# Kernel optimization log

Measured on AMD Instinct MI355X. Metric: run time of the kernel, lower is better.

## Reference

```python
import jax, jax.numpy as jnp
import numpy as np

B, H_IMG, W_IMG = 2, 192, 192
DIM, HEADS, WS, SHIFT = 192, 6, 8, 4
MLP_HID = 4 * DIM
EPS = 1e-5


def _rel_pos_index(ws):
    coords = np.stack(np.meshgrid(np.arange(ws), np.arange(ws), indexing='ij'))  # (2, ws, ws)
    cf = coords.reshape(2, -1)
    rel = (cf[:, :, None] - cf[:, None, :]).transpose(1, 2, 0)  # (ww, ww, 2)
    rel[:, :, 0] += ws - 1
    rel[:, :, 1] += ws - 1
    rel[:, :, 0] *= 2 * ws - 1
    return jnp.asarray(rel.sum(-1))  # (ww, ww) int


def _attn_mask(h, w, ws, shift):
    img = np.zeros((h, w))
    cnt = 0
    for hs in (slice(0, -ws), slice(-ws, -shift), slice(-shift, None)):
        for wsl in (slice(0, -ws), slice(-ws, -shift), slice(-shift, None)):
            img[hs, wsl] = cnt
            cnt += 1
    mw = img.reshape(h // ws, ws, w // ws, ws).transpose(0, 2, 1, 3).reshape(-1, ws * ws)
    am = mw[:, None, :] - mw[:, :, None]
    return jnp.asarray(np.where(am != 0, -100.0, 0.0), dtype=jnp.float32)


def setup_inputs() -> dict:
    key = jax.random.key(0)
    ks = jax.random.split(key, 16)
    n = H_IMG * W_IMG
    std = 0.02
    inp = {
        'x_left': jax.random.normal(ks[0], (B, n, DIM), jnp.float32),
        'x_right': jax.random.normal(ks[1], (B, n, DIM), jnp.float32),
        'd_left': jax.random.uniform(ks[2], (B, H_IMG, W_IMG), jnp.float32) * 8.0,
        'd_right': jax.random.uniform(ks[3], (B, H_IMG, W_IMG), jnp.float32) * 8.0,
        'norm1_g': jnp.ones((DIM,), jnp.float32),
        'norm1_b': jnp.zeros((DIM,), jnp.float32),
        'q_w': jax.random.normal(ks[4], (DIM, DIM), jnp.float32) * std,
        'q_b': jnp.zeros((DIM,), jnp.float32),
        'kv_w': jax.random.normal(ks[5], (DIM, 2 * DIM), jnp.float32) * std,
        'kv_b': jnp.zeros((2 * DIM,), jnp.float32),
        'proj_w': jax.random.normal(ks[6], (DIM, DIM), jnp.float32) * std,
        'proj_b': jnp.zeros((DIM,), jnp.float32),
        'rel_bias_table': jax.random.normal(ks[7], ((2 * WS - 1) ** 2, HEADS), jnp.float32) * std,
        'norm2_g': jnp.ones((DIM,), jnp.float32),
        'norm2_b': jnp.zeros((DIM,), jnp.float32),
        'fc1_w': jax.random.normal(ks[8], (DIM, MLP_HID), jnp.float32) * std,
        'fc1_b': jnp.zeros((MLP_HID,), jnp.float32),
        'fc2_w': jax.random.normal(ks[9], (MLP_HID, DIM), jnp.float32) * std,
        'fc2_b': jnp.zeros((DIM,), jnp.float32),
        'h': H_IMG,
        'w': W_IMG,
    }
    return inp


def _forward(x_left, x_right, d_left, d_right,
             norm1_g, norm1_b, q_w, q_b, kv_w, kv_b, proj_w, proj_b,
             rel_bias_table, norm2_g, norm2_b, fc1_w, fc1_b, fc2_w, fc2_b,
             h, w):
    b, n, c = x_left.shape
    ws, shift, heads = WS, SHIFT, HEADS
    hd = c // heads
    scale = hd ** -0.5
    ww = ws * ws
    nW = (h // ws) * (w // ws)

    rel_idx = _rel_pos_index(ws)
    # (heads, ww, ww) gathered relative-position bias
    bias = rel_bias_table[rel_idx.reshape(-1)].reshape(ww, ww, heads).transpose(2, 0, 1)
    mask = _attn_mask(h, w, ws, shift)  # (nW, ww, ww)

    coords_w = jnp.arange(w, dtype=jnp.float32)[None, None, :]
    r2l = jnp.clip(coords_w + 0.5 - d_left, 0.0, None).astype(jnp.int32)
    l2r = jnp.clip(coords_w + 0.5 + d_right, None, float(w - 1)).astype(jnp.int32)

    def ln(x, g, bt):
        mu = x.mean(-1, keepdims=True)
        var = ((x - mu) ** 2).mean(-1, keepdims=True)
        return (x - mu) / jnp.sqrt(var + EPS) * g + bt

    sc_l, sc_r = x_left, x_right
    xl = ln(x_left, norm1_g, norm1_b).reshape(b, h, w, c)
    xr = ln(x_right, norm1_g, norm1_b).reshape(b, h, w, c)
    # epipolar gather along width
    xl_sel = jnp.take_along_axis(xl, l2r[..., None], axis=2)
    xr_sel = jnp.take_along_axis(xr, r2l[..., None], axis=2)

    def shift_f(x):
        return jnp.roll(x, (-shift, -shift), axis=(1, 2))

    def part(x):  # window partition -> (b*nW, ww, c)
        x = x.reshape(b, h // ws, ws, w // ws, ws, c).transpose(0, 1, 3, 2, 4, 5)
        return x.reshape(-1, ww, c)

    xlw, xrw = part(shift_f(xl)), part(shift_f(xr))
    xlsw, xrsw = part(shift_f(xl_sel)), part(shift_f(xr_sel))

    def win_attn(xq, xkv):
        B_ = xq.shape[0]
        q = (xq @ q_w + q_b).reshape(B_, ww, heads, hd).transpose(0, 2, 1, 3) * scale
        kv = (xkv @ kv_w + kv_b).reshape(B_, ww, 2, heads, hd).transpose(2, 0, 3, 1, 4)
        k, v = kv[0], kv[1]
        a = jnp.einsum('bhqd,bhkd->bhqk', q, k) + bias[None]
        a = a.reshape(B_ // nW, nW, heads, ww, ww) + mask[None, :, None]
        a = jax.nn.softmax(a.reshape(B_, heads, ww, ww), axis=-1)
        o = jnp.einsum('bhqk,bhkd->bqhd', a, v).reshape(B_, ww, c)
        return o @ proj_w + proj_b, a

    xlT, a_r2l = win_attn(xlw, xrsw)
    xrT, a_l2r = win_attn(xrw, xlsw)

    def m_relax(M, p=2):  # sum over +-p shifts along the query axis
        out = M
        for i in range(1, p + 1):
            out = out + jnp.pad(M[:, :, :-i, :], ((0, 0), (0, 0), (i, 0), (0, 0)))
            out = out + jnp.pad(M[:, :, i:, :], ((0, 0), (0, 0), (0, i), (0, 0)))
        return out

    m_l = jnp.einsum('bhik,bhki->bhi', m_relax(a_r2l), a_l2r)
    m_r = jnp.einsum('bhik,bhki->bhi', m_relax(a_l2r), a_r2l)
    m_l = jax.lax.stop_gradient(jnp.tanh(5.0 * m_l.transpose(0, 2, 1)[..., None]))  # (B_, ww, heads, 1)
    m_r = jax.lax.stop_gradient(jnp.tanh(5.0 * m_r.transpose(0, 2, 1)[..., None]))

    def fuse(x_orig, x_t, m):
        B_ = x_orig.shape[0]
        xo = x_orig.reshape(B_, ww, heads, hd)
        xt = x_t.reshape(B_, ww, heads, hd)
        return (xo * (1.0 - m) + xt * m).reshape(B_, ww, c)

    xlT = fuse(xlw, xlT, m_l)
    xrT = fuse(xrw, xrT, m_r)

    def rev(win):  # window reverse + roll back
        x = win.reshape(b, h // ws, w // ws, ws, ws, c).transpose(0, 1, 3, 2, 4, 5).reshape(b, h, w, c)
        return jnp.roll(x, (shift, shift), axis=(1, 2))

    xl_out = sc_l + rev(xlT).reshape(b, n, c)
    xr_out = sc_r + rev(xrT).reshape(b, n, c)

    def mlp(x):
        return jax.nn.gelu(x @ fc1_w + fc1_b, approximate=False) @ fc2_w + fc2_b

    xl_out = xl_out + mlp(ln(xl_out, norm2_g, norm2_b))
    xr_out = xr_out + mlp(ln(xr_out, norm2_g, norm2_b))
    return xl_out, xr_out


def reference(x_left, x_right, d_left, d_right,
              norm1_g, norm1_b, q_w, q_b, kv_w, kv_b, proj_w, proj_b,
              rel_bias_table, norm2_g, norm2_b, fc1_w, fc1_b, fc2_w, fc2_b,
              h, w):
    return _forward(x_left, x_right, d_left, d_right,
                    norm1_g, norm1_b, q_w, q_b, kv_w, kv_b, proj_w, proj_b,
                    rel_bias_table, norm2_g, norm2_b, fc1_w, fc1_b, fc2_w, fc2_b,
                    h, w)
```

## Files before the change

kernel.cpp:

```cpp
#include <hip/hip_runtime.h>
#include <hip/hip_bf16.h>

#define BB 2
#define HH 192
#define WIMG 192
#define CC 192
#define NHEADS 6
#define HD 32
#define NTOK (HH*WIMG)
#define NWX 24
#define NWIN 576
#define BWIN (BB*NWIN)
#define MLPH 768
#define EPS_ 1e-5f
#define NSIDE_TOK (BB*NTOK)

typedef __attribute__((ext_vector_type(8))) short bf16x8;
typedef __attribute__((ext_vector_type(4))) float f32x4;

#define GLOBAL_AS __attribute__((address_space(1)))
#define LDS_AS __attribute__((address_space(3)))
__device__ __forceinline__ void gll16(const void* g, void* l) {
    __builtin_amdgcn_global_load_lds((const GLOBAL_AS unsigned int*)g,
                                     (LDS_AS unsigned int*)l, 16, 0, 0);
}

__device__ __forceinline__ unsigned short f2bf(float f) {
    __hip_bfloat16 h = __float2bfloat16(f);
    return *reinterpret_cast<unsigned short*>(&h);
}
__device__ __forceinline__ float bfu(unsigned short u) {
    return __uint_as_float(((unsigned int)u) << 16);
}
__device__ __forceinline__ float gelu_fast(float x) {
    float z = 1.5957691216f*(x + 0.044715f*x*x*x);
    float e = __expf(z);
    float t = 1.0f - 2.0f/(e + 1.0f);
    return 0.5f*x*(1.0f + t);
}
__device__ __forceinline__ int tokof(int b, int wi, int wj, int p) {
    int rh = wi*8 + (p>>3), rw = wj*8 + (p&7);
    int i = rh + 4; if (i >= HH) i -= HH;
    int j = rw + 4; if (j >= WIMG) j -= WIMG;
    return b*NTOK + i*WIMG + j;
}

__global__ __launch_bounds__(256) void ln1_kernel(
    const float* __restrict__ xl, const float* __restrict__ xr,
    const float* __restrict__ g, const float* __restrict__ bta,
    __hip_bfloat16* __restrict__ xln_all)
{
    int token = blockIdx.x*4 + (threadIdx.x >> 6);
    int lane = threadIdx.x & 63;
    const float* src;
    __hip_bfloat16* dst;
    if (token < NSIDE_TOK) { src = xl + (size_t)token*CC; dst = xln_all + (size_t)token*CC; }
    else { int t2 = token - NSIDE_TOK; src = xr + (size_t)t2*CC; dst = xln_all + (size_t)token*CC; }
    float v0 = src[lane], v1 = src[lane+64], v2 = src[lane+128];
    float s = v0+v1+v2;
    float q = v0*v0 + v1*v1 + v2*v2;
    #pragma unroll
    for (int m = 32; m; m >>= 1) { s += __shfl_xor(s, m, 64); q += __shfl_xor(q, m, 64); }
    float mu = s * (1.0f/CC);
    float inv = rsqrtf(fmaxf(q*(1.0f/CC) - mu*mu, 0.0f) + EPS_);
    dst[lane]     = __float2bfloat16((v0-mu)*inv*g[lane]     + bta[lane]);
    dst[lane+64]  = __float2bfloat16((v1-mu)*inv*g[lane+64]  + bta[lane+64]);
    dst[lane+128] = __float2bfloat16((v2-mu)*inv*g[lane+128] + bta[lane+128]);
}

__global__ __launch_bounds__(256) void map_kernel(
    const float* __restrict__ d_left, const float* __restrict__ d_right,
    int* __restrict__ map)
{
    int gid = blockIdx.x*256 + threadIdx.x;
    int side = (gid >= NSIDE_TOK) ? 1 : 0;
    int row = gid - side*NSIDE_TOK;
    int j = row % WIMG;
    float d = side ? d_right[row] : d_left[row];
    int jj;
    if (!side) { float f = (float)j + 0.5f - d; f = fmaxf(f, 0.f); jj = (int)f; }
    else       { float f = (float)j + 0.5f + d; f = fminf(f, 191.f); jj = (int)f; }
    map[gid] = (side ? 0 : NSIDE_TOK) + row - j + jj;
}

__global__ __launch_bounds__(256) void conv_w_kernel(
    const float* __restrict__ q_w, const float* __restrict__ kv_w,
    const float* __restrict__ proj_w, const float* __restrict__ fc1_w,
    const float* __restrict__ fc2_w,
    __hip_bfloat16* __restrict__ q_wf, __hip_bfloat16* __restrict__ kv_wf,
    __hip_bfloat16* __restrict__ proj_f, __hip_bfloat16* __restrict__ W1f,
    __hip_bfloat16* __restrict__ W2f)
{
    int idx = blockIdx.x*256 + threadIdx.x;
    if (idx < 36864) {
        int j = idx & 7, lane = (idx>>3) & 63, fr = idx>>9;
        int ct = fr % 12, ks = fr / 12;
        int n = ct*16 + (lane&15), k = ks*32 + (lane>>4)*8 + j;
        q_wf[idx] = __float2bfloat16(q_w[(size_t)k*192 + n]);
    } else if (idx < 110592) {
        int i2 = idx - 36864;
        int j = i2 & 7, lane = (i2>>3) & 63, fr = i2>>9;
        int ct = fr % 24, ks = fr / 24;
        int n = ct*16 + (lane&15), k = ks*32 + (lane>>4)*8 + j;
        kv_wf[i2] = __float2bfloat16(kv_w[(size_t)k*384 + n]);
    } else if (idx < 147456) {
        int i2 = idx - 110592;
        int j = i2 & 7, lane = (i2>>3) & 63, fr = i2>>9;
        int ct = fr % 12, h = fr / 12;
        int n = ct*16 + (lane&15), k = h*32 + (lane>>4)*8 + j;
        proj_f[i2] = __float2bfloat16(proj_w[(size_t)k*192 + n]);
    } else if (idx < 294912) {
        int i2 = idx - 147456;
        int j = i2 & 7, lane = (i2>>3) & 63, fr = i2>>9;
        int ct = fr & 1, ks = (fr>>1) % 6, cc2 = fr / 12;
        int n = cc2*32 + ct*16 + (lane&15), k = ks*32 + (lane>>4)*8 + j;
        W1f[i2] = __float2bfloat16(fc1_w[(size_t)k*MLPH + n]);
    } else {
        int i2 = idx - 294912;
        int j = i2 & 7, lane = (i2>>3) & 63, fr = i2>>9;
        int ct = fr % 12, ks = (fr/12) % 2, cc = fr / 24;
        int n = ct*16 + (lane&15), k = cc*64 + ks*32 + (lane>>4)*8 + j;
        W2f[i2] = __float2bfloat16(fc2_w[(size_t)k*192 + n]);
    }
}

__global__ __launch_bounds__(256) void bias_setup_kernel(
    const float* __restrict__ table, float* __restrict__ bias_glob)
{
    int idx = blockIdx.x*256 + threadIdx.x;
    int h = idx >> 12, rem = idx & 4095;
    int q = rem >> 6, k = rem & 63;
    int qy = q>>3, qx = q&7, ky = k>>3, kx = k&7;
    int ridx = (qy-ky+7)*15 + (qx-kx+7);
    bias_glob[idx] = table[ridx*NHEADS + h];
}

template<int NT>
__global__ __launch_bounds__(256) void proj_gemm_kernel(
    const __hip_bfloat16* __restrict__ in, const __hip_bfloat16* __restrict__ Wf,
    const float* __restrict__ bias, const int* __restrict__ map,
    __hip_bfloat16* __restrict__ outp, float scale)
{
    __shared__ unsigned short wst[2][NT*512];
    const int tid = threadIdx.x, lane = tid & 63, w = tid >> 6;
    const int r16 = lane & 15, kg = lane >> 4, w16 = w*16;
    const size_t baserow = (size_t)blockIdx.x * 64;
    const int row = (int)baserow + w16 + r16;
    const size_t arow = map ? (size_t)map[row] : (size_t)row;

    bf16x8 aReg[6];
    #pragma unroll
    for (int ks = 0; ks < 6; ++ks)
        aReg[ks] = *reinterpret_cast<const bf16x8*>(in + arow*CC + ks*32 + kg*8);

    const char* wsrc = (const char*)Wf;
    const int soff = w*1024 + lane*16;
    #pragma unroll
    for (int i = 0; i < NT/4; ++i)
        gll16(wsrc + i*4096 + soff, (char*)wst[0] + i*4096 + w*1024);

    f32x4 acc[NT];
    #pragma unroll
    for (int ct = 0; ct < NT; ++ct) { float bv = bias[ct*16+r16]; acc[ct] = (f32x4){bv,bv,bv,bv}; }

    #pragma unroll
    for (int ks = 0; ks < 6; ++ks) {
        __syncthreads();
        if (ks < 5) {
            const char* s2 = wsrc + (size_t)(ks+1)*NT*1024;
            #pragma unroll
            for (int i = 0; i < NT/4; ++i)
                gll16(s2 + i*4096 + soff, (char*)wst[(ks+1)&1] + i*4096 + w*1024);
        }
        #pragma unroll
        for (int ct = 0; ct < NT; ++ct) {
            bf16x8 bb = *reinterpret_cast<const bf16x8*>(wst[ks&1] + ct*512 + lane*8);
            acc[ct] = __builtin_amdgcn_mfma_f32_16x16x32_bf16(aReg[ks], bb, acc[ct], 0, 0, 0);
        }
    }
    const int ldo = NT*16;
    #pragma unroll
    for (int ct = 0; ct < NT; ++ct)
        #pragma unroll
        for (int r = 0; r < 4; ++r)
            outp[(baserow + w16 + kg*4 + r)*ldo + ct*16 + r16] =
                __float2bfloat16(acc[ct][r] * scale);
}

__global__ __launch_bounds__(128) void attn_pm_kernel(
    const __hip_bfloat16* __restrict__ Qglob,
    const __hip_bfloat16* __restrict__ KVglob,
    const float* __restrict__ bias_glob,
    __hip_bfloat16* __restrict__ Og,
    float* __restrict__ mg)
{
    __shared__ unsigned short Pl[2][64*72];
    __shared__ unsigned short Vl[2][32*72];
    const int tid = threadIdx.x, lane = tid & 63, s = tid >> 6;
    const int r16 = lane & 15, kg = lane >> 4;
    const int bid = blockIdx.x;
    const int wd = bid / NHEADS, h = bid % NHEADS;
    const int b = wd / NWIN, win = wd % NWIN;
    const int wi = win / NWX, wj = win % NWX;
    const bool edge_i = (wi == NWX-1), edge_j = (wj == NWX-1);

    const __hip_bfloat16* Qs  = Qglob  + (size_t)s*NSIDE_TOK*CC;
    const __hip_bfloat16* KVs = KVglob + (size_t)s*NSIDE_TOK*(2*CC);

    int tokQ[4];
    #pragma unroll
    for (int mi = 0; mi < 4; ++mi) tokQ[mi] = tokof(b, wi, wj, mi*16 + r16);
    const int tokV = tokof(b, wi, wj, lane);

    unsigned short* P = Pl[s];
    unsigned short* V = Vl[s];

    {
        bf16x8 vv[4];
        #pragma unroll
        for (int dg = 0; dg < 4; ++dg)
            vv[dg] = *reinterpret_cast<const bf16x8*>(
                KVs + (size_t)tokV*(2*CC) + CC + h*HD + dg*8);
        #pragma unroll
        for (int dg = 0; dg < 4; ++dg)
            #pragma unroll
            for (int jj = 0; jj < 8; ++jj)
                V[(dg*8+jj)*72 + lane] = (unsigned short)vv[dg][jj];
    }

    bf16x8 aQ[4], bK[4];
    #pragma unroll
    for (int mi = 0; mi < 4; ++mi)
        aQ[mi] = *reinterpret_cast<const bf16x8*>(
            Qs + (size_t)tokQ[mi]*CC + h*HD + kg*8);
    #pragma unroll
    for (int ni = 0; ni < 4; ++ni)
        bK[ni] = *reinterpret_cast<const bf16x8*>(
            KVs + (size_t)tokQ[ni]*(2*CC) + h*HD + kg*8);
    f32x4 S[4][4];
    #pragma unroll
    for (int mi = 0; mi < 4; ++mi)
        #pragma unroll
        for (int ni = 0; ni < 4; ++ni)
            S[mi][ni] = __builtin_amdgcn_mfma_f32_16x16x32_bf16(
                aQ[mi], bK[ni], (f32x4){0.f,0.f,0.f,0.f}, 0, 0, 0);

    #pragma unroll
    for (int mi = 0; mi < 4; ++mi)
        #pragma unroll
        for (int ni = 0; ni < 4; ++ni)
            #pragma unroll
            for (int rr = 0; rr < 4; ++rr) {
                int q = mi*16 + kg*4 + rr, k = ni*16 + r16;
                float bm = bias_glob[h*4096 + q*64 + k];
                int qy = q>>3, qx = q&7, ky = k>>3, kx = k&7;
                bool msk = (edge_i && ((qy<4) != (ky<4))) ||
                           (edge_j && ((qx<4) != (kx<4)));
                S[mi][ni][rr] += bm + (msk ? -100.0f : 0.0f);
            }

    float mx[4][4], sm[4][4];
    #pragma unroll
    for (int mi = 0; mi < 4; ++mi)
        #pragma unroll
        for (int rr = 0; rr < 4; ++rr)
            mx[mi][rr] = fmaxf(fmaxf(S[mi][0][rr], S[mi][1][rr]),
                               fmaxf(S[mi][2][rr], S[mi][3][rr]));
    #pragma unroll
    for (int m = 1; m <= 8; m <<= 1)
        #pragma unroll
        for (int mi = 0; mi < 4; ++mi)
            #pragma unroll
            for (int rr = 0; rr < 4; ++rr)
                mx[mi][rr] = fmaxf(mx[mi][rr], __shfl_xor(mx[mi][rr], m, 64));
    #pragma unroll
    for (int mi = 0; mi < 4; ++mi)
        #pragma unroll
        for (int rr = 0; rr < 4; ++rr) sm[mi][rr] = 0.f;
    #pragma unroll
    for (int mi = 0; mi < 4; ++mi)
        #pragma unroll
        for (int ni = 0; ni < 4; ++ni)
            #pragma unroll
            for (int rr = 0; rr < 4; ++rr) {
                S[mi][ni][rr] = __expf(S[mi][ni][rr] - mx[mi][rr]);
                sm[mi][rr] += S[mi][ni][rr];
            }
    #pragma unroll
    for (int m = 1; m <= 8; m <<= 1)
        #pragma unroll
        for (int mi = 0; mi < 4; ++mi)
            #pragma unroll
            for (int rr = 0; rr < 4; ++rr)
                sm[mi][rr] += __shfl_xor(sm[mi][rr], m, 64);
    #pragma unroll
    for (int mi = 0; mi < 4; ++mi)
        #pragma unroll
        for (int rr = 0; rr < 4; ++rr) sm[mi][rr] = 1.0f / sm[mi][rr];

    #pragma unroll
    for (int mi = 0; mi < 4; ++mi)
        #pragma unroll
        for (int ni = 0; ni < 4; ++ni)
            #pragma unroll
            for (int rr = 0; rr < 4; ++rr)
                P[(mi*16 + kg*4 + rr)*72 + ni*16 + r16] =
                    f2bf(S[mi][ni][rr] * sm[mi][rr]);

    {
        f32x4 O[4][2];
        #pragma unroll
        for (int mi = 0; mi < 4; ++mi)
            #pragma unroll
            for (int dt = 0; dt < 2; ++dt) O[mi][dt] = (f32x4){0.f,0.f,0.f,0.f};
        #pragma unroll
        for (int ks = 0; ks < 2; ++ks) {
            bf16x8 aP[4], bV[2];
            #pragma unroll
            for (int mi = 0; mi < 4; ++mi)
                aP[mi] = *reinterpret_cast<const bf16x8*>(
                    P + (mi*16 + r16)*72 + ks*32 + kg*8);
            #pragma unroll
            for (int dt = 0; dt < 2; ++dt)
                bV[dt] = *reinterpret_cast<const bf16x8*>(
                    V + (dt*16 + r16)*72 + ks*32 + kg*8);
            #pragma unroll
            for (int mi = 0; mi < 4; ++mi)
                #pragma unroll
                for (int dt = 0; dt < 2; ++dt)
                    O[mi][dt] = __builtin_amdgcn_mfma_f32_16x16x32_bf16(
                        aP[mi], bV[dt], O[mi][dt], 0, 0, 0);
        }
        __hip_bfloat16* ob = Og + ((size_t)(s*BWIN + wd)*64)*CC + h*HD;
        #pragma unroll
        for (int mi = 0; mi < 4; ++mi)
            #pragma unroll
            for (int dt = 0; dt < 2; ++dt)
                #pragma unroll
                for (int rr = 0; rr < 4; ++rr)
                    ob[(size_t)(mi*16 + kg*4 + rr)*CC + dt*16 + r16] =
                        __float2bfloat16(O[mi][dt][rr]);
    }

    __syncthreads();

    {
        const unsigned short* Pa = Pl[s];
        const unsigned short* Pb = Pl[s^1];
        const int i = lane;
        const int s0 = (i >= 2) ? -2 : -i;
        const int s1 = (i <= 61) ? 2 : 63 - i;
        float acc = 0.f;
        for (int k = 0; k < 64; k += 2) {
            float pb0 = bfu(Pb[k*72 + i]);
            float pb1 = bfu(Pb[(k+1)*72 + i]);
            float a0 = 0.f, a1 = 0.f;
            for (int ss = s0; ss <= s1; ++ss) {
                unsigned int pr = *reinterpret_cast<const unsigned int*>(
                    &Pa[(i+ss)*72 + k]);
                a0 += bfu((unsigned short)(pr & 0xffff));
                a1 += bfu((unsigned short)(pr >> 16));
            }
            acc += a0*pb0 + a1*pb1;
        }
        float e = __expf(10.0f * acc);
        mg[((size_t)(s*BWIN + wd)*NHEADS + h)*64 + i] = 1.0f - 2.0f/(e + 1.0f);
    }
}

__global__ __launch_bounds__(256) void projfuse_kernel(
    const __hip_bfloat16* __restrict__ Og,
    const __hip_bfloat16* __restrict__ proj_f,
    const float* __restrict__ proj_b,
    const float* __restrict__ mg,
    const __hip_bfloat16* __restrict__ xln_all,
    const float* __restrict__ x_left, const float* __restrict__ x_right,
    const float* __restrict__ g2, const float* __restrict__ b2,
    float* __restrict__ out, __hip_bfloat16* __restrict__ xln2)
{
    __shared__ unsigned short wst[2][12*512];
    const int tid = threadIdx.x, lane = tid & 63, w = tid >> 6;
    const int r16 = lane & 15, kg = lane >> 4, w16 = w*16;
    const int bid = blockIdx.x;
    const int s = bid / BWIN, wd = bid % BWIN;
    const int b = wd / NWIN, win = wd % NWIN;
    const int wi = win / NWX, wj = win % NWX;

    const size_t orow = (size_t)(s*BWIN + wd)*64 + w16 + r16;
    bf16x8 aReg[6];
    #pragma unroll
    for (int ks = 0; ks < 6; ++ks)
        aReg[ks] = *reinterpret_cast<const bf16x8*>(Og + orow*CC + ks*32 + kg*8);

    const char* wsrc = (const char*)proj_f;
    const int soff = w*1024 + lane*16;
    #pragma unroll
    for (int i = 0; i < 3; ++i)
        gll16(wsrc + i*4096 + soff, (char*)wst[0] + i*4096 + w*1024);

    f32x4 acc[12];
    #pragma unroll
    for (int ct = 0; ct < 12; ++ct) { float bv = proj_b[ct*16+r16]; acc[ct] = (f32x4){bv,bv,bv,bv}; }

    #pragma unroll
    for (int ks = 0; ks < 6; ++ks) {
        __syncthreads();
        if (ks < 5) {
            const char* s2 = wsrc + (size_t)(ks+1)*12288;
            #pragma unroll
            for (int i = 0; i < 3; ++i)
                gll16(s2 + i*4096 + soff, (char*)wst[(ks+1)&1] + i*4096 + w*1024);
        }
        #pragma unroll
        for (int ct = 0; ct < 12; ++ct) {
            bf16x8 bb = *reinterpret_cast<const bf16x8*>(wst[ks&1] + ct*512 + lane*8);
            acc[ct] = __builtin_amdgcn_mfma_f32_16x16x32_bf16(aReg[ks], bb, acc[ct], 0, 0, 0);
        }
    }

    int tk[4];
    #pragma unroll
    for (int rr = 0; rr < 4; ++rr) tk[rr] = tokof(b, wi, wj, w16 + kg*4 + rr);
    const float* xo_s = s ? x_right : x_left;
    const __hip_bfloat16* xw_s = xln_all + (size_t)s*NSIDE_TOK*CC;
    float* out_s = out + (size_t)s*NSIDE_TOK*CC;
    __hip_bfloat16* xln2_s = xln2 + (size_t)s*NSIDE_TOK*CC;
    const float* mrow = mg + (size_t)(s*BWIN + wd)*NHEADS*64;

    float g2c[12], b2c[12];
    #pragma unroll
    for (int ct = 0; ct < 12; ++ct) {
        g2c[ct] = g2[ct*16 + r16];
        b2c[ct] = b2[ct*16 + r16];
    }

    #pragma unroll
    for (int ct = 0; ct < 12; ++ct) {
        int col = ct*16 + r16;
        int h = ct >> 1;
        #pragma unroll
        for (int rr = 0; rr < 4; ++rr) {
            int q = w16 + kg*4 + rr;
            size_t tt = (size_t)tk[rr];
            float m = mrow[h*64 + q];
            float xw = __bfloat162float(xw_s[tt*CC + col]);
            float p = acc[ct][rr];
            float val = xo_s[tt*CC + col] + xw + (p - xw)*m;
            out_s[tt*CC + col] = val;
            acc[ct][rr] = val;
        }
    }

    #pragma unroll
    for (int rr = 0; rr < 4; ++rr) {
        float sum = 0.f, sq = 0.f;
        #pragma unroll
        for (int ct = 0; ct < 12; ++ct) {
            float v = acc[ct][rr];
            sum += v; sq += v*v;
        }
        #pragma unroll
        for (int m = 1; m <= 8; m <<= 1) {
            sum += __shfl_xor(sum, m, 64);
            sq  += __shfl_xor(sq,  m, 64);
        }
        float mu = sum * (1.0f/CC);
        float inv = rsqrtf(fmaxf(sq*(1.0f/CC) - mu*mu, 0.0f) + EPS_);
        size_t tt = (size_t)tk[rr];
        #pragma unroll
        for (int ct = 0; ct < 12; ++ct) {
            unsigned short uv = f2bf((acc[ct][rr]-mu)*inv*g2c[ct] + b2c[ct]);
            *reinterpret_cast<unsigned short*>(&xln2_s[tt*CC + ct*16 + r16]) = uv;
        }
    }
}

__global__ __launch_bounds__(512) void mlp_mfma_kernel(
    float* __restrict__ out, const __hip_bfloat16* __restrict__ xln2,
    const __hip_bfloat16* __restrict__ W1f, const float* __restrict__ fc1_b,
    const __hip_bfloat16* __restrict__ W2f, const float* __restrict__ fc2_b)
{
    __shared__ unsigned short hbuf[2][64*72];
    __shared__ unsigned short wst[2][6144];
    const int tid  = threadIdx.x;
    const int lane = tid & 63;
    const int w    = tid >> 6;
    const int tg   = w >> 2;
    const int w4   = w & 3;
    const int r16 = lane & 15, kg = lane >> 4, w16 = w4*16;
    const size_t base = (size_t)blockIdx.x * 128 * CC + (size_t)tg * 64 * CC;

    bf16x8 aReg[6];
    #pragma unroll
    for (int ks = 0; ks < 6; ++ks)
        aReg[ks] = *reinterpret_cast<const bf16x8*>(
            xln2 + base + (size_t)(w16 + r16)*CC + ks*32 + kg*8);

    const char* W1c = (const char*)W1f;
    const char* W2c = (const char*)W2f;
    const int soff = w*4096 + lane*16;
    const int doff = w*4096;
    unsigned short* hb = hbuf[tg];

    if (w < 3) {
        #pragma unroll
        for (int i = 0; i < 4; ++i)
            gll16(W1c + i*1024 + soff, (char*)wst[0] + i*1024 + doff);
    }

    f32x4 acc2[12];
    #pragma unroll
    for (int i = 0; i < 12; ++i) acc2[i] = (f32x4){0.f,0.f,0.f,0.f};

    for (int cc = 0; cc < 12; ++cc) {
        f32x4 acc1[4];
        __builtin_amdgcn_s_barrier();
        if (w < 3) {
            const char* s2 = W1c + (size_t)(2*cc+1)*12288;
            #pragma unroll
            for (int i = 0; i < 4; ++i)
                gll16(s2 + i*1024 + soff, (char*)wst[1] + i*1024 + doff);
        }
        asm volatile("s_waitcnt vmcnt(4)" ::: "memory");
        __builtin_amdgcn_s_barrier();
        #pragma unroll
        for (int c2 = 0; c2 < 2; ++c2) {
            float bv = fc1_b[cc*64 + c2*16 + r16];
            acc1[c2] = (f32x4){bv,bv,bv,bv};
        }
        #pragma unroll
        for (int ks = 0; ks < 6; ++ks)
            #pragma unroll
            for (int c2 = 0; c2 < 2; ++c2) {
                bf16x8 bw = *reinterpret_cast<const bf16x8*>(wst[0] + (ks*2+c2)*512 + lane*8);
                acc1[c2] = __builtin_amdgcn_mfma_f32_16x16x32_bf16(aReg[ks], bw, acc1[c2], 0, 0, 0);
            }
        __builtin_amdgcn_s_barrier();
        if (w < 3) {
            const char* s2 = W2c + (size_t)(2*cc)*12288;
            #pragma unroll
            for (int i = 0; i < 4; ++i)
                gll16(s2 + i*1024 + soff, (char*)wst[0] + i*1024 + doff);
        }
        asm volatile("s_waitcnt vmcnt(4)" ::: "memory");
        __builtin_amdgcn_s_barrier();
        #pragma unroll
        for (int c2 = 0; c2 < 2; ++c2) {
            float bv = fc1_b[cc*64 + 32 + c2*16 + r16];
            acc1[2+c2] = (f32x4){bv,bv,bv,bv};
        }
        #pragma unroll
        for (int ks = 0; ks < 6; ++ks)
            #pragma unroll
            for (int c2 = 0; c2 < 2; ++c2) {
                bf16x8 bw = *reinterpret_cast<const bf16x8*>(wst[1] + (ks*2+c2)*512 + lane*8);
                acc1[2+c2] = __builtin_amdgcn_mfma_f32_16x16x32_bf16(aReg[ks], bw, acc1[2+c2], 0, 0, 0);
            }
        #pragma unroll
        for (int ct = 0; ct < 4; ++ct)
            #pragma unroll
            for (int r = 0; r < 4; ++r)
                hb[(w16 + kg*4 + r)*72 + ct*16 + r16] = f2bf(gelu_fast(acc1[ct][r]));
        __builtin_amdgcn_s_barrier();
        if (w < 3) {
            const char* s2 = W2c + (size_t)(2*cc+1)*12288;
            #pragma unroll
            for (int i = 0; i < 4; ++i)
                gll16(s2 + i*1024 + soff, (char*)wst[1] + i*1024 + doff);
        }
        asm volatile("s_waitcnt vmcnt(4)" ::: "memory");
        __builtin_amdgcn_s_barrier();
        {
            bf16x8 aP = *reinterpret_cast<const bf16x8*>(hb + (w16+r16)*72 + kg*8);
            #pragma unroll
            for (int ct = 0; ct < 12; ++ct) {
                bf16x8 bw = *reinterpret_cast<const bf16x8*>(wst[0] + ct*512 + lane*8);
                acc2[ct] = __builtin_amdgcn_mfma_f32_16x16x32_bf16(aP, bw, acc2[ct], 0, 0, 0);
            }
        }
        __builtin_amdgcn_s_barrier();
        if (cc < 11) {
            if (w < 3) {
                const char* s2 = W1c + (size_t)(2*cc+2)*12288;
                #pragma unroll
                for (int i = 0; i < 4; ++i)
                    gll16(s2 + i*1024 + soff, (char*)wst[0] + i*1024 + doff);
            }
            asm volatile("s_waitcnt vmcnt(4)" ::: "memory");
        } else {
            asm volatile("s_waitcnt vmcnt(0)" ::: "memory");
        }
        __builtin_amdgcn_s_barrier();
        {
            bf16x8 aP = *reinterpret_cast<const bf16x8*>(hb + (w16+r16)*72 + 32 + kg*8);
            #pragma unroll
            for (int ct = 0; ct < 12; ++ct) {
                bf16x8 bw = *reinterpret_cast<const bf16x8*>(wst[1] + ct*512 + lane*8);
                acc2[ct] = __builtin_amdgcn_mfma_f32_16x16x32_bf16(aP, bw, acc2[ct], 0, 0, 0);
            }
        }
    }

    #pragma unroll
    for (int ct = 0; ct < 12; ++ct) {
        int col = ct*16 + r16;
        float bv = fc2_b[col];
        #pragma unroll
        for (int r = 0; r < 4; ++r) {
            size_t idx = base + (size_t)(w16 + kg*4 + r)*CC + col;
            out[idx] = out[idx] + acc2[ct][r] + bv;
        }
    }
}

extern "C" void kernel_launch(void* const* d_in, const int* in_sizes, int n_in,
                              void* d_out, int out_size, void* d_ws, size_t ws_size,
                              hipStream_t stream)
{
    (void)in_sizes; (void)n_in; (void)out_size; (void)ws_size;
    const float* x_left  = (const float*)d_in[0];
    const float* x_right = (const float*)d_in[1];
    const float* d_left  = (const float*)d_in[2];
    const float* d_right = (const float*)d_in[3];
    const float* n1g = (const float*)d_in[4];
    const float* n1b = (const float*)d_in[5];
    const float* q_w = (const float*)d_in[6];
    const float* q_b = (const float*)d_in[7];
    const float* kv_w = (const float*)d_in[8];
    const float* kv_b = (const float*)d_in[9];
    const float* proj_w = (const float*)d_in[10];
    const float* proj_b = (const float*)d_in[11];
    const float* bias_table = (const float*)d_in[12];
    const float* n2g = (const float*)d_in[13];
    const float* n2b = (const float*)d_in[14];
    const float* fc1_w = (const float*)d_in[15];
    const float* fc1_b = (const float*)d_in[16];
    const float* fc2_w = (const float*)d_in[17];
    const float* fc2_b = (const float*)d_in[18];
    float* out = (float*)d_out;

    char* ws = (char*)d_ws;
    __hip_bfloat16* xln_all  = (__hip_bfloat16*)(ws);
    __hip_bfloat16* Qg       = (__hip_bfloat16*)(ws + 56623104);
    __hip_bfloat16* KVg      = (__hip_bfloat16*)(ws + 113246208);
    __hip_bfloat16* xln2     = (__hip_bfloat16*)(ws + 113246208);
    __hip_bfloat16* q_wf     = (__hip_bfloat16*)(ws + 226492416);
    __hip_bfloat16* kv_wf    = (__hip_bfloat16*)(ws + 226566144);
    __hip_bfloat16* proj_f   = (__hip_bfloat16*)(ws + 226713600);
    __hip_bfloat16* W1f      = (__hip_bfloat16*)(ws + 226787328);
    __hip_bfloat16* W2f      = (__hip_bfloat16*)(ws + 227082240);
    float*          bias_g   = (float*)         (ws + 227377152);
    __hip_bfloat16* Og       = (__hip_bfloat16*)(ws + 227770368);
    int*            map      = (int*)           (ws + 284393472);
    float*          mg       = (float*)         (ws + 284983296);

    ln1_kernel<<<(2*NSIDE_TOK)/4, 256, 0, stream>>>(x_left, x_right, n1g, n1b, xln_all);

    conv_w_kernel<<<1728, 256, 0, stream>>>(q_w, kv_w, proj_w, fc1_w, fc2_w,
                                            q_wf, kv_wf, proj_f, W1f, W2f);
    bias_setup_kernel<<<96, 256, 0, stream>>>(bias_table, bias_g);
    map_kernel<<<(2*NSIDE_TOK)/256, 256, 0, stream>>>(d_left, d_right, map);

    proj_gemm_kernel<24><<<(2*NSIDE_TOK)/64, 256, 0, stream>>>(
        xln_all, kv_wf, kv_b, map, KVg, 1.0f);
    proj_gemm_kernel<12><<<(2*NSIDE_TOK)/64, 256, 0, stream>>>(
        xln_all, q_wf, q_b, nullptr, Qg, 0.17677669529663687f);

    attn_pm_kernel<<<BWIN*NHEADS, 128, 0, stream>>>(Qg, KVg, bias_g, Og, mg);

    projfuse_kernel<<<2*BWIN, 256, 0, stream>>>(
        Og, proj_f, proj_b, mg, xln_all, x_left, x_right, n2g, n2b, out, xln2);

    mlp_mfma_kernel<<<(2*NSIDE_TOK)/128, 512, 0, stream>>>(
        out, xln2, W1f, fc1_b, W2f, fc2_b);
}
```

Measured before the change: 536.9 us.

## Merge setup kernels, widen Q-proj and projfuse blocks, restructure attention loads

Folds the weight conversion, bias-table expansion and disparity map kernels into one setup launch to cut launch overhead. Adds a 512-thread Q projection GEMM and widens projfuse to 512 threads, so one staged weight tile in LDS serves two row groups. In both, only three waves issue the LDS loads and explicit vmcnt waits with split barriers replace __syncthreads. The attention kernel interleaves K loads with the MFMAs to lower register pressure, at the cost of being more sensitive to load latency.

```diff
diff --git a/kernel.cpp b/kernel.cpp
--- a/kernel.cpp
+++ b/kernel.cpp
@@ -68,28 +68,15 @@
     dst[lane+128] = __float2bfloat16((v2-mu)*inv*g[lane+128] + bta[lane+128]);
 }
 
-__global__ __launch_bounds__(256) void map_kernel(
-    const float* __restrict__ d_left, const float* __restrict__ d_right,
-    int* __restrict__ map)
-{
-    int gid = blockIdx.x*256 + threadIdx.x;
-    int side = (gid >= NSIDE_TOK) ? 1 : 0;
-    int row = gid - side*NSIDE_TOK;
-    int j = row % WIMG;
-    float d = side ? d_right[row] : d_left[row];
-    int jj;
-    if (!side) { float f = (float)j + 0.5f - d; f = fmaxf(f, 0.f); jj = (int)f; }
-    else       { float f = (float)j + 0.5f + d; f = fminf(f, 191.f); jj = (int)f; }
-    map[gid] = (side ? 0 : NSIDE_TOK) + row - j + jj;
-}
-
-__global__ __launch_bounds__(256) void conv_w_kernel(
+__global__ __launch_bounds__(256) void setup_kernel(
     const float* __restrict__ q_w, const float* __restrict__ kv_w,
     const float* __restrict__ proj_w, const float* __restrict__ fc1_w,
-    const float* __restrict__ fc2_w,
+    const float* __restrict__ fc2_w, const float* __restrict__ table,
+    const float* __restrict__ d_left, const float* __restrict__ d_right,
     __hip_bfloat16* __restrict__ q_wf, __hip_bfloat16* __restrict__ kv_wf,
     __hip_bfloat16* __restrict__ proj_f, __hip_bfloat16* __restrict__ W1f,
-    __hip_bfloat16* __restrict__ W2f)
+    __hip_bfloat16* __restrict__ W2f, float* __restrict__ bias_glob,
+    int* __restrict__ map)
 {
     int idx = blockIdx.x*256 + threadIdx.x;
     if (idx < 36864) {
@@ -115,24 +102,30 @@
         int ct = fr & 1, ks = (fr>>1) % 6, cc2 = fr / 12;
         int n = cc2*32 + ct*16 + (lane&15), k = ks*32 + (lane>>4)*8 + j;
         W1f[i2] = __float2bfloat16(fc1_w[(size_t)k*MLPH + n]);
-    } else {
+    } else if (idx < 442368) {
         int i2 = idx - 294912;
         int j = i2 & 7, lane = (i2>>3) & 63, fr = i2>>9;
         int ct = fr % 12, ks = (fr/12) % 2, cc = fr / 24;
         int n = ct*16 + (lane&15), k = cc*64 + ks*32 + (lane>>4)*8 + j;
         W2f[i2] = __float2bfloat16(fc2_w[(size_t)k*192 + n]);
-    }
-}
-
-__global__ __launch_bounds__(256) void bias_setup_kernel(
-    const float* __restrict__ table, float* __restrict__ bias_glob)
-{
-    int idx = blockIdx.x*256 + threadIdx.x;
-    int h = idx >> 12, rem = idx & 4095;
-    int q = rem >> 6, k = rem & 63;
-    int qy = q>>3, qx = q&7, ky = k>>3, kx = k&7;
-    int ridx = (qy-ky+7)*15 + (qx-kx+7);
-    bias_glob[idx] = table[ridx*NHEADS + h];
+    } else if (idx < 466944) {
+        int i3 = idx - 442368;
+        int h = i3 >> 12, rem = i3 & 4095;
+        int q = rem >> 6, k = rem & 63;
+        int qy = q>>3, qx = q&7, ky = k>>3, kx = k&7;
+        int ridx = (qy-ky+7)*15 + (qx-kx+7);
+        bias_glob[i3] = table[ridx*NHEADS + h];
+    } else {
+        int gid = idx - 466944;
+        int side = (gid >= NSIDE_TOK) ? 1 : 0;
+        int row = gid - side*NSIDE_TOK;
+        int j = row % WIMG;
+        float d = side ? d_right[row] : d_left[row];
+        int jj;
+        if (!side) { float f = (float)j + 0.5f - d; f = fmaxf(f, 0.f); jj = (int)f; }
+        else       { float f = (float)j + 0.5f + d; f = fminf(f, 191.f); jj = (int)f; }
+        map[gid] = (side ? 0 : NSIDE_TOK) + row - j + jj;
+    }
 }
 
 template<int NT>
@@ -184,6 +177,64 @@
         #pragma unroll
         for (int r = 0; r < 4; ++r)
             outp[(baserow + w16 + kg*4 + r)*ldo + ct*16 + r16] =
+                __float2bfloat16(acc[ct][r] * scale);
+}
+
+__global__ __launch_bounds__(512) void proj_gemm12x2_kernel(
+    const __hip_bfloat16* __restrict__ in, const __hip_bfloat16* __restrict__ Wf,
+    const float* __restrict__ bias, __hip_bfloat16* __restrict__ outp, float scale)
+{
+    __shared__ unsigned short wst[2][12*512];
+    const int tid = threadIdx.x, lane = tid & 63, w = tid >> 6;
+    const int tg = w >> 2, w4 = w & 3;
+    const int r16 = lane & 15, kg = lane >> 4, w16 = w4*16;
+    const size_t baserow = (size_t)blockIdx.x * 128 + (size_t)tg * 64;
+    const size_t arow = baserow + w16 + r16;
+
+    bf16x8 aReg[6];
+    #pragma unroll
+    for (int ks = 0; ks < 6; ++ks)
+        aReg[ks] = *reinterpret_cast<const bf16x8*>(in + arow*CC + ks*32 + kg*8);
+
+    const char* wsrc = (const char*)Wf;
+    const int soff = w*4096 + lane*16;
+    const int doff = w*4096;
+    if (w < 3) {
+        #pragma unroll
+        for (int i = 0; i < 4; ++i)
+            gll16(wsrc + i*1024 + soff, (char*)wst[0] + i*1024 + doff);
+    }
+
+    f32x4 acc[12];
+    #pragma unroll
+    for (int ct = 0; ct < 12; ++ct) { float bv = bias[ct*16+r16]; acc[ct] = (f32x4){bv,bv,bv,bv}; }
+
+    #pragma unroll
+    for (int ks = 0; ks < 6; ++ks) {
+        __builtin_amdgcn_s_barrier();
+        if (ks < 5) {
+            if (w < 3) {
+                const char* s2 = wsrc + (size_t)(ks+1)*12288;
+                #pragma unroll
+                for (int i = 0; i < 4; ++i)
+                    gll16(s2 + i*1024 + soff, (char*)wst[(ks+1)&1] + i*1024 + doff);
+            }
+            asm volatile("s_waitcnt vmcnt(4)" ::: "memory");
+        } else {
+            asm volatile("s_waitcnt vmcnt(0)" ::: "memory");
+        }
+        __builtin_amdgcn_s_barrier();
+        #pragma unroll
+        for (int ct = 0; ct < 12; ++ct) {
+            bf16x8 bb = *reinterpret_cast<const bf16x8*>(wst[ks&1] + ct*512 + lane*8);
+            acc[ct] = __builtin_amdgcn_mfma_f32_16x16x32_bf16(aReg[ks], bb, acc[ct], 0, 0, 0);
+        }
+    }
+    #pragma unroll
+    for (int ct = 0; ct < 12; ++ct)
+        #pragma unroll
+        for (int r = 0; r < 4; ++r)
+            outp[(baserow + w16 + kg*4 + r)*192 + ct*16 + r16] =
                 __float2bfloat16(acc[ct][r] * scale);
 }
 
@@ -215,35 +266,30 @@
     unsigned short* P = Pl[s];
     unsigned short* V = Vl[s];
 
-    {
-        bf16x8 vv[4];
-        #pragma unroll
-        for (int dg = 0; dg < 4; ++dg)
-            vv[dg] = *reinterpret_cast<const bf16x8*>(
-                KVs + (size_t)tokV*(2*CC) + CC + h*HD + dg*8);
-        #pragma unroll
-        for (int dg = 0; dg < 4; ++dg)
-            #pragma unroll
-            for (int jj = 0; jj < 8; ++jj)
-                V[(dg*8+jj)*72 + lane] = (unsigned short)vv[dg][jj];
-    }
-
-    bf16x8 aQ[4], bK[4];
+    #pragma unroll
+    for (int dg = 0; dg < 4; ++dg) {
+        bf16x8 vv = *reinterpret_cast<const bf16x8*>(
+            KVs + (size_t)tokV*(2*CC) + CC + h*HD + dg*8);
+        #pragma unroll
+        for (int jj = 0; jj < 8; ++jj)
+            V[(dg*8+jj)*72 + lane] = (unsigned short)vv[jj];
+    }
+
+    bf16x8 aQ[4];
     #pragma unroll
     for (int mi = 0; mi < 4; ++mi)
         aQ[mi] = *reinterpret_cast<const bf16x8*>(
             Qs + (size_t)tokQ[mi]*CC + h*HD + kg*8);
-    #pragma unroll
-    for (int ni = 0; ni < 4; ++ni)
-        bK[ni] = *reinterpret_cast<const bf16x8*>(
+    f32x4 S[4][4];
+    #pragma unroll
+    for (int ni = 0; ni < 4; ++ni) {
+        bf16x8 bK = *reinterpret_cast<const bf16x8*>(
             KVs + (size_t)tokQ[ni]*(2*CC) + h*HD + kg*8);
-    f32x4 S[4][4];
-    #pragma unroll
-    for (int mi = 0; mi < 4; ++mi)
-        #pragma unroll
-        for (int ni = 0; ni < 4; ++ni)
+        #pragma unroll
+        for (int mi = 0; mi < 4; ++mi)
             S[mi][ni] = __builtin_amdgcn_mfma_f32_16x16x32_bf16(
-                aQ[mi], bK[ni], (f32x4){0.f,0.f,0.f,0.f}, 0, 0, 0);
+                aQ[mi], bK, (f32x4){0.f,0.f,0.f,0.f}, 0, 0, 0);
+    }
 
     #pragma unroll
     for (int mi = 0; mi < 4; ++mi)
@@ -368,7 +414,7 @@
     }
 }
 
-__global__ __launch_bounds__(256) void projfuse_kernel(
+__global__ __launch_bounds__(512) void projfuse_kernel(
     const __hip_bfloat16* __restrict__ Og,
     const __hip_bfloat16* __restrict__ proj_f,
     const float* __restrict__ proj_b,
@@ -380,23 +426,27 @@
 {
     __shared__ unsigned short wst[2][12*512];
     const int tid = threadIdx.x, lane = tid & 63, w = tid >> 6;
-    const int r16 = lane & 15, kg = lane >> 4, w16 = w*16;
-    const int bid = blockIdx.x;
-    const int s = bid / BWIN, wd = bid % BWIN;
+    const int tg = w >> 2, w4 = w & 3;
+    const int r16 = lane & 15, kg = lane >> 4, w16 = w4*16;
+    const int u = blockIdx.x*2 + tg;
+    const int s = u / BWIN, wd = u % BWIN;
     const int b = wd / NWIN, win = wd % NWIN;
     const int wi = win / NWX, wj = win % NWX;
 
-    const size_t orow = (size_t)(s*BWIN + wd)*64 + w16 + r16;
+    const size_t orow = (size_t)u*64 + w16 + r16;
     bf16x8 aReg[6];
     #pragma unroll
     for (int ks = 0; ks < 6; ++ks)
         aReg[ks] = *reinterpret_cast<const bf16x8*>(Og + orow*CC + ks*32 + kg*8);
 
     const char* wsrc = (const char*)proj_f;
-    const int soff = w*1024 + lane*16;
-    #pragma unroll
-    for (int i = 0; i < 3; ++i)
-        gll16(wsrc + i*4096 + soff, (char*)wst[0] + i*4096 + w*1024);
+    const int soff = w*4096 + lane*16;
+    const int doff = w*4096;
+    if (w < 3) {
+        #pragma unroll
+        for (int i = 0; i < 4; ++i)
+            gll16(wsrc + i*1024 + soff, (char*)wst[0] + i*1024 + doff);
+    }
 
     f32x4 acc[12];
     #pragma unroll
@@ -404,13 +454,19 @@
 
     #pragma unroll
     for (int ks = 0; ks < 6; ++ks) {
-        __syncthreads();
+        __builtin_amdgcn_s_barrier();
         if (ks < 5) {
-            const char* s2 = wsrc + (size_t)(ks+1)*12288;
-            #pragma unroll
-            for (int i = 0; i < 3; ++i)
-                gll16(s2 + i*4096 + soff, (char*)wst[(ks+1)&1] + i*4096 + w*1024);
-        }
+            if (w < 3) {
+                const char* s2 = wsrc + (size_t)(ks+1)*12288;
+                #pragma unroll
+                for (int i = 0; i < 4; ++i)
+                    gll16(s2 + i*1024 + soff, (char*)wst[(ks+1)&1] + i*1024 + doff);
+            }
+            asm volatile("s_waitcnt vmcnt(4)" ::: "memory");
+        } else {
+            asm volatile("s_waitcnt vmcnt(0)" ::: "memory");
+        }
+        __builtin_amdgcn_s_barrier();
         #pragma unroll
         for (int ct = 0; ct < 12; ++ct) {
             bf16x8 bb = *reinterpret_cast<const bf16x8*>(wst[ks&1] + ct*512 + lane*8);
@@ -425,7 +481,7 @@
     const __hip_bfloat16* xw_s = xln_all + (size_t)s*NSIDE_TOK*CC;
     float* out_s = out + (size_t)s*NSIDE_TOK*CC;
     __hip_bfloat16* xln2_s = xln2 + (size_t)s*NSIDE_TOK*CC;
-    const float* mrow = mg + (size_t)(s*BWIN + wd)*NHEADS*64;
+    const float* mrow = mg + (size_t)u*NHEADS*64;
 
     float g2c[12], b2c[12];
     #pragma unroll
@@ -656,19 +712,18 @@
 
     ln1_kernel<<<(2*NSIDE_TOK)/4, 256, 0, stream>>>(x_left, x_right, n1g, n1b, xln_all);
 
-    conv_w_kernel<<<1728, 256, 0, stream>>>(q_w, kv_w, proj_w, fc1_w, fc2_w,
-                                            q_wf, kv_wf, proj_f, W1f, W2f);
-    bias_setup_kernel<<<96, 256, 0, stream>>>(bias_table, bias_g);
-    map_kernel<<<(2*NSIDE_TOK)/256, 256, 0, stream>>>(d_left, d_right, map);
+    setup_kernel<<<2400, 256, 0, stream>>>(
+        q_w, kv_w, proj_w, fc1_w, fc2_w, bias_table, d_left, d_right,
+        q_wf, kv_wf, proj_f, W1f, W2f, bias_g, map);
 
     proj_gemm_kernel<24><<<(2*NSIDE_TOK)/64, 256, 0, stream>>>(
         xln_all, kv_wf, kv_b, map, KVg, 1.0f);
-    proj_gemm_kernel<12><<<(2*NSIDE_TOK)/64, 256, 0, stream>>>(
-        xln_all, q_wf, q_b, nullptr, Qg, 0.17677669529663687f);
+    proj_gemm12x2_kernel<<<(2*NSIDE_TOK)/128, 512, 0, stream>>>(
+        xln_all, q_wf, q_b, Qg, 0.17677669529663687f);
 
     attn_pm_kernel<<<BWIN*NHEADS, 128, 0, stream>>>(Qg, KVg, bias_g, Og, mg);
 
-    projfuse_kernel<<<2*BWIN, 256, 0, stream>>>(
+    projfuse_kernel<<<BWIN, 512, 0, stream>>>(
         Og, proj_f, proj_b, mg, xln_all, x_left, x_right, n2g, n2b, out, xln2);
 
     mlp_mfma_kernel<<<(2*NSIDE_TOK)/128, 512, 0, stream>>>(
```

After: 547.4 us. No clear change (+1.9%).
